# Performance work log

Hardware: AMD Instinct MI355X
Metric: run time of the kernel (lower is better)

Reference implementation:

```python
import jax, jax.numpy as jnp
import numpy as np

T, B, D, H = 1024, 512, 128, 256


def setup_inputs() -> dict:
    key = jax.random.key(0)
    k0, k1, k2, k3, k4, k5 = jax.random.split(key, 6)
    data = jax.random.normal(k0, (T, B, D), dtype=jnp.float32)
    # ragged lengths in [1, T]; masked recurrence == packed-sequence semantics
    lengths = jax.random.randint(k1, (B,), 1, T + 1, dtype=jnp.int32)
    s_ih = 1.0 / np.sqrt(D)
    s_hh = 1.0 / np.sqrt(H)
    ih_w = jax.random.uniform(k2, (H, D), minval=-s_ih, maxval=s_ih, dtype=jnp.float32)
    ih_b = jax.random.uniform(k3, (H,), minval=-s_ih, maxval=s_ih, dtype=jnp.float32)
    hh_w = jax.random.uniform(k4, (2 * H, H), minval=-s_hh, maxval=s_hh, dtype=jnp.float32)
    hh_b = jax.random.uniform(k5, (2 * H,), minval=-s_hh, maxval=s_hh, dtype=jnp.float32)
    return {"data": data, "ih_w": ih_w, "ih_b": ih_b, "hh_w": hh_w, "hh_b": hh_b, "lengths": lengths}


def reference(data, ih_w, ih_b, hh_w, hh_b, lengths):
    # data: [T, B, D]; masked update replicates packed-sequence 'first size rows' semantics
    Tn, Bn, _ = data.shape
    Hn = ih_w.shape[0]

    def step(hidden, inp):
        x_t, t = inp
        hid = hidden @ hh_w.T + hh_b                    # [B, 2H]
        alpha, h = jnp.split(hid, 2, axis=1)
        alpha = jax.nn.sigmoid(alpha)
        h = (jnp.exp2(alpha * h) - 1.0) / alpha + alpha  # soft-exp gate
        new_hidden = jnp.tanh(x_t @ ih_w.T + ih_b + h)   # [B, H]
        valid = (t < lengths)[:, None]
        return jnp.where(valid, new_hidden, hidden), None

    h0 = jnp.zeros((Bn, Hn), dtype=data.dtype)
    hidden, _ = jax.lax.scan(step, h0, (data, jnp.arange(Tn)))
    return hidden[None]  # [1, B, H], matching hidden.unsqueeze(0)
```

## Files before the change

kernel.cpp:

```cpp
#include <hip/hip_runtime.h>


#define BB 512
#define DD 128
#define HH 256

typedef __attribute__((ext_vector_type(8))) short bf16x8;
typedef __attribute__((ext_vector_type(4))) float f32x4;

static __device__ __forceinline__ short f2bf(float f) {
    unsigned u = __float_as_uint(f);
    u += 0x7FFFu + ((u >> 16) & 1u);
    return (short)(u >> 16);
}
static __device__ __forceinline__ float bf2f(short s) {
    return __uint_as_float(((unsigned)(unsigned short)s) << 16);
}
static __device__ __forceinline__ bf16x8 pack8(const float4 a, const float4 b) {
    bf16x8 v;
    v[0] = f2bf(a.x); v[1] = f2bf(a.y); v[2] = f2bf(a.z); v[3] = f2bf(a.w);
    v[4] = f2bf(b.x); v[5] = f2bf(b.y); v[6] = f2bf(b.z); v[7] = f2bf(b.w);
    return v;
}

__global__ __launch_bounds__(512, 2)
void rnn_fused(const float* __restrict__ data, const float* __restrict__ ih_w,
               const float* __restrict__ ih_b, const float* __restrict__ hh_w,
               const float* __restrict__ hh_b, const int* __restrict__ lengths,
               float* __restrict__ out)
{
    const int g    = blockIdx.x;
    const int tid  = threadIdx.x;
    const int w    = tid >> 6;
    const int lane = tid & 63;
    const int col  = lane & 15;
    const int quad = lane >> 4;

    __shared__ short hbuf[2][32][4][8];
    __shared__ short dbuf[2][2][DD];

    bf16x8 whh[4][8];
    #pragma unroll
    for (int s = 0; s < 2; ++s)
        #pragma unroll
        for (int j = 0; j < 2; ++j) {
            const int wrow = s*HH + 32*w + 16*j + col;
            const float* src = hh_w + wrow * HH;
            #pragma unroll
            for (int i = 0; i < 8; ++i) {
                const float4 a = *(const float4*)(src + i*32 + quad*8);
                const float4 b = *(const float4*)(src + i*32 + quad*8 + 4);
                whh[s*2 + j][i] = pack8(a, b);
            }
        }
    bf16x8 wih[2][4];
    #pragma unroll
    for (int j = 0; j < 2; ++j) {
        const int wrow = 32*w + 16*j + col;
        const float* src = ih_w + wrow * DD;
        #pragma unroll
        for (int i = 0; i < 4; ++i) {
            const float4 a = *(const float4*)(src + i*32 + quad*8);
            const float4 b = *(const float4*)(src + i*32 + quad*8 + 4);
            wih[j][i] = pack8(a, b);
        }
    }

    float bA[2], bH[2], bX[2];
    #pragma unroll
    for (int j = 0; j < 2; ++j) {
        bA[j] = hh_b[      32*w + 16*j + col];
        bH[j] = hh_b[HH  + 32*w + 16*j + col];
        bX[j] = ih_b[      32*w + 16*j + col];
    }

    const int L0 = lengths[2*g];
    const int L1 = lengths[2*g + 1];
    const int Lmax = (L0 > L1) ? L0 : L1;

    for (int idx = tid; idx < 32*4*8; idx += 512)
        ((short*)hbuf[0])[idx] = 0;
    if (tid < 256)
        ((short*)dbuf[0])[tid] = f2bf(data[(size_t)(2*g) * DD + tid]);
    float vstage = 0.f;
    if (tid < 256 && 1 < Lmax)
        vstage = data[((size_t)1 * BB + 2*g) * DD + tid];
    __syncthreads();

    float  nh[2][2] = {{0.f,0.f},{0.f,0.f}};
    bf16x8 af[4] = {};
    bf16x8 dh[4] = {};

    const bool act = (col < 4);

    for (int t = 0; t < Lmax; ++t) {
        const int p = t & 1;

        if (tid < 256 && t + 1 < Lmax)
            ((short*)dbuf[1 - p])[tid] = f2bf(vstage);
        float vnew = 0.f;
        if (tid < 256 && t + 2 < Lmax)
            vnew = data[((size_t)(t+2) * BB + 2*g) * DD + tid];

        f32x4 racc[4];
        #pragma unroll
        for (int j = 0; j < 2; ++j) {
            f32x4 va = {bA[j], bA[j], 0.f, 0.f}; racc[j]     = va;
            f32x4 vh = {bH[j], bH[j], 0.f, 0.f}; racc[2 + j] = vh;
        }
        #pragma unroll
        for (int half = 0; half < 2; ++half) {
            if (act) {
                #pragma unroll
                for (int i = 0; i < 4; ++i)
                    af[i] = *(const bf16x8*)
                        &hbuf[p][(half*4 + i)*4 + quad][col][0];
            }
            #pragma unroll
            for (int i = 0; i < 4; ++i)
                #pragma unroll
                for (int tt = 0; tt < 4; ++tt)
                    racc[tt] = __builtin_amdgcn_mfma_f32_16x16x32_bf16(
                        af[i], whh[tt][half*4 + i], racc[tt], 0, 0, 0);
        }

        if (act && col < 2) {
            #pragma unroll
            for (int i = 0; i < 4; ++i)
                dh[i] = *(const bf16x8*)&dbuf[p][col][i*32 + quad*8];
        }
        f32x4 xacc[2];
        #pragma unroll
        for (int j = 0; j < 2; ++j) {
            f32x4 v = {bX[j], bX[j], bX[j], bX[j]}; xacc[j] = v;
        }
        #pragma unroll
        for (int i = 0; i < 4; ++i)
            #pragma unroll
            for (int j = 0; j < 2; ++j)
                xacc[j] = __builtin_amdgcn_mfma_f32_16x16x32_bf16(
                    dh[i], wih[j][i], xacc[j], 0, 0, 0);

        #pragma unroll
        for (int j = 0; j < 2; ++j) {
            #pragma unroll
            for (int r = 0; r < 2; ++r) {
                const float a   = racc[j][r]     + racc[j][2 + r];
                const float hv  = racc[2 + j][r] + racc[2 + j][2 + r];
                const float e   = __builtin_amdgcn_exp2f(a * -1.4426950408889634f);
                const float inv = 1.0f + e;
                const float al  = __builtin_amdgcn_rcpf(inv);
                const float pp  = __builtin_amdgcn_exp2f(al * hv);
                const float gg  = (pp - 1.0f) * inv + al;
                const float u   = xacc[j][r] + gg;
                const float t2  = __builtin_amdgcn_exp2f(u * 2.8853900817779268f);
                const float th  = 1.0f - 2.0f * __builtin_amdgcn_rcpf(1.0f + t2);
                const int   Lr  = r ? L1 : L0;
                const float v   = (t < Lr) ? th : nh[j][r];
                nh[j][r] = v;
                if (quad == 0) {
                    const int   c  = 32*w + 16*j + col;
                    const short hi = f2bf(v);
                    const short lo = f2bf(v - bf2f(hi));
                    hbuf[1 - p][c >> 3][r    ][c & 7] = hi;
                    hbuf[1 - p][c >> 3][2 + r][c & 7] = lo;
                }
            }
        }

        vstage = vnew;
        __syncthreads();
    }

    if (quad == 0) {
        #pragma unroll
        for (int j = 0; j < 2; ++j)
            #pragma unroll
            for (int r = 0; r < 2; ++r)
                out[(size_t)(2*g + r) * HH + 32*w + 16*j + col] = nh[j][r];
    }
}

extern "C" void kernel_launch(void* const* d_in, const int* in_sizes, int n_in,
                              void* d_out, int out_size, void* d_ws, size_t ws_size,
                              hipStream_t stream) {
    const float* data    = (const float*)d_in[0];
    const float* ih_w    = (const float*)d_in[1];
    const float* ih_b    = (const float*)d_in[2];
    const float* hh_w    = (const float*)d_in[3];
    const float* hh_b    = (const float*)d_in[4];
    const int*   lengths = (const int*)d_in[5];
    float* out = (float*)d_out;

    (void)in_sizes; (void)n_in; (void)out_size; (void)d_ws; (void)ws_size;

    rnn_fused<<<dim3(BB / 2), dim3(512), 0, stream>>>(
        data, ih_w, ih_b, hh_w, hh_b, lengths, out);
}
```

Before: 1.474 ms.

## Split hidden columns across 16 waves per block to shorten per-step MFMA chain

Doubles the block size to 1024 threads so each wave owns 16 hidden columns instead of 32. This halves the per-wave recurrent and input MFMA counts and the gate math on the serial time-step critical path. Register weight storage per wave is halved, and biases are now added after accumulation. The cost is a barrier across more waves each step and higher register pressure on occupancy under the 1024,4 launch bound.

New measurement: 1.364 ms. 7.5% less time.

```diff
diff --git a/kernel.cpp b/kernel.cpp
--- a/kernel.cpp
+++ b/kernel.cpp
@@ -23,7 +23,7 @@
     return v;
 }
 
-__global__ __launch_bounds__(512, 2)
+__global__ __launch_bounds__(1024, 4)
 void rnn_fused(const float* __restrict__ data, const float* __restrict__ ih_w,
                const float* __restrict__ ih_b, const float* __restrict__ hh_w,
                const float* __restrict__ hh_b, const int* __restrict__ lengths,
@@ -39,46 +39,39 @@
     __shared__ short hbuf[2][32][4][8];
     __shared__ short dbuf[2][2][DD];
 
-    bf16x8 whh[4][8];
+    bf16x8 whh[2][8];
     #pragma unroll
-    for (int s = 0; s < 2; ++s)
+    for (int s = 0; s < 2; ++s) {
+        const int wrow = s*HH + 16*w + col;
+        const float* src = hh_w + wrow * HH;
         #pragma unroll
-        for (int j = 0; j < 2; ++j) {
-            const int wrow = s*HH + 32*w + 16*j + col;
-            const float* src = hh_w + wrow * HH;
-            #pragma unroll
-            for (int i = 0; i < 8; ++i) {
-                const float4 a = *(const float4*)(src + i*32 + quad*8);
-                const float4 b = *(const float4*)(src + i*32 + quad*8 + 4);
-                whh[s*2 + j][i] = pack8(a, b);
-            }
+        for (int i = 0; i < 8; ++i) {
+            const float4 a = *(const float4*)(src + i*32 + quad*8);
+            const float4 b = *(const float4*)(src + i*32 + quad*8 + 4);
+            whh[s][i] = pack8(a, b);
         }
-    bf16x8 wih[2][4];
-    #pragma unroll
-    for (int j = 0; j < 2; ++j) {
-        const int wrow = 32*w + 16*j + col;
+    }
+    bf16x8 wih[4];
+    {
+        const int wrow = 16*w + col;
         const float* src = ih_w + wrow * DD;
         #pragma unroll
         for (int i = 0; i < 4; ++i) {
             const float4 a = *(const float4*)(src + i*32 + quad*8);
             const float4 b = *(const float4*)(src + i*32 + quad*8 + 4);
-            wih[j][i] = pack8(a, b);
+            wih[i] = pack8(a, b);
         }
     }
 
-    float bA[2], bH[2], bX[2];
-    #pragma unroll
-    for (int j = 0; j < 2; ++j) {
-        bA[j] = hh_b[      32*w + 16*j + col];
-        bH[j] = hh_b[HH  + 32*w + 16*j + col];
-        bX[j] = ih_b[      32*w + 16*j + col];
-    }
+    const float bA = hh_b[      16*w + col];
+    const float bH = hh_b[HH  + 16*w + col];
+    const float bX = ih_b[      16*w + col];
 
     const int L0 = lengths[2*g];
     const int L1 = lengths[2*g + 1];
     const int Lmax = (L0 > L1) ? L0 : L1;
 
-    for (int idx = tid; idx < 32*4*8; idx += 512)
+    for (int idx = tid; idx < 32*4*8; idx += 1024)
         ((short*)hbuf[0])[idx] = 0;
     if (tid < 256)
         ((short*)dbuf[0])[tid] = f2bf(data[(size_t)(2*g) * DD + tid]);
@@ -87,11 +80,11 @@
         vstage = data[((size_t)1 * BB + 2*g) * DD + tid];
     __syncthreads();
 
-    float  nh[2][2] = {{0.f,0.f},{0.f,0.f}};
-    bf16x8 af[4] = {};
-    bf16x8 dh[4] = {};
+    float  nh[2] = {0.f, 0.f};
+    bf16x8 frag[4] = {};
 
-    const bool act = (col < 4);
+    const bool acth = (col < 4);
+    const bool actd = (col < 2);
 
     for (int t = 0; t < Lmax; ++t) {
         const int p = t & 1;
@@ -102,69 +95,55 @@
         if (tid < 256 && t + 2 < Lmax)
             vnew = data[((size_t)(t+2) * BB + 2*g) * DD + tid];
 
-        f32x4 racc[4];
-        #pragma unroll
-        for (int j = 0; j < 2; ++j) {
-            f32x4 va = {bA[j], bA[j], 0.f, 0.f}; racc[j]     = va;
-            f32x4 vh = {bH[j], bH[j], 0.f, 0.f}; racc[2 + j] = vh;
-        }
+        f32x4 racc[2] = {{0.f,0.f,0.f,0.f},{0.f,0.f,0.f,0.f}};
         #pragma unroll
         for (int half = 0; half < 2; ++half) {
-            if (act) {
+            if (acth) {
                 #pragma unroll
                 for (int i = 0; i < 4; ++i)
-                    af[i] = *(const bf16x8*)
+                    frag[i] = *(const bf16x8*)
                         &hbuf[p][(half*4 + i)*4 + quad][col][0];
             }
             #pragma unroll
             for (int i = 0; i < 4; ++i)
                 #pragma unroll
-                for (int tt = 0; tt < 4; ++tt)
-                    racc[tt] = __builtin_amdgcn_mfma_f32_16x16x32_bf16(
-                        af[i], whh[tt][half*4 + i], racc[tt], 0, 0, 0);
+                for (int s = 0; s < 2; ++s)
+                    racc[s] = __builtin_amdgcn_mfma_f32_16x16x32_bf16(
+                        frag[i], whh[s][half*4 + i], racc[s], 0, 0, 0);
         }
 
-        if (act && col < 2) {
+        if (actd) {
             #pragma unroll
             for (int i = 0; i < 4; ++i)
-                dh[i] = *(const bf16x8*)&dbuf[p][col][i*32 + quad*8];
+                frag[i] = *(const bf16x8*)&dbuf[p][col][i*32 + quad*8];
         }
-        f32x4 xacc[2];
-        #pragma unroll
-        for (int j = 0; j < 2; ++j) {
-            f32x4 v = {bX[j], bX[j], bX[j], bX[j]}; xacc[j] = v;
-        }
+        f32x4 xacc = {0.f, 0.f, 0.f, 0.f};
         #pragma unroll
         for (int i = 0; i < 4; ++i)
-            #pragma unroll
-            for (int j = 0; j < 2; ++j)
-                xacc[j] = __builtin_amdgcn_mfma_f32_16x16x32_bf16(
-                    dh[i], wih[j][i], xacc[j], 0, 0, 0);
+            xacc = __builtin_amdgcn_mfma_f32_16x16x32_bf16(
+                frag[i], wih[i], xacc, 0, 0, 0);
 
         #pragma unroll
-        for (int j = 0; j < 2; ++j) {
-            #pragma unroll
-            for (int r = 0; r < 2; ++r) {
-                const float a   = racc[j][r]     + racc[j][2 + r];
-                const float hv  = racc[2 + j][r] + racc[2 + j][2 + r];
-                const float e   = __builtin_amdgcn_exp2f(a * -1.4426950408889634f);
-                const float inv = 1.0f + e;
-                const float al  = __builtin_amdgcn_rcpf(inv);
-                const float pp  = __builtin_amdgcn_exp2f(al * hv);
-                const float gg  = (pp - 1.0f) * inv + al;
-                const float u   = xacc[j][r] + gg;
-                const float t2  = __builtin_amdgcn_exp2f(u * 2.8853900817779268f);
-                const float th  = 1.0f - 2.0f * __builtin_amdgcn_rcpf(1.0f + t2);
-                const int   Lr  = r ? L1 : L0;
-                const float v   = (t < Lr) ? th : nh[j][r];
-                nh[j][r] = v;
-                if (quad == 0) {
-                    const int   c  = 32*w + 16*j + col;
-                    const short hi = f2bf(v);
-                    const short lo = f2bf(v - bf2f(hi));
-                    hbuf[1 - p][c >> 3][r    ][c & 7] = hi;
-                    hbuf[1 - p][c >> 3][2 + r][c & 7] = lo;
-                }
+        for (int r = 0; r < 2; ++r) {
+            const float a   = racc[0][r] + racc[0][2 + r] + bA;
+            const float hv  = racc[1][r] + racc[1][2 + r] + bH;
+            const float e   = __builtin_amdgcn_exp2f(a * -1.4426950408889634f);
+            const float inv = 1.0f + e;
+            const float al  = __builtin_amdgcn_rcpf(inv);
+            const float pp  = __builtin_amdgcn_exp2f(al * hv);
+            const float gg  = (pp - 1.0f) * inv + al;
+            const float u   = xacc[r] + bX + gg;
+            const float t2  = __builtin_amdgcn_exp2f(u * 2.8853900817779268f);
+            const float th  = 1.0f - 2.0f * __builtin_amdgcn_rcpf(1.0f + t2);
+            const int   Lr  = r ? L1 : L0;
+            const float v   = (t < Lr) ? th : nh[r];
+            nh[r] = v;
+            if (quad == 0) {
+                const int   c  = 16*w + col;
+                const short hi = f2bf(v);
+                const short lo = f2bf(v - bf2f(hi));
+                hbuf[1 - p][c >> 3][r    ][c & 7] = hi;
+                hbuf[1 - p][c >> 3][2 + r][c & 7] = lo;
             }
         }
 
@@ -174,10 +153,8 @@
 
     if (quad == 0) {
         #pragma unroll
-        for (int j = 0; j < 2; ++j)
-            #pragma unroll
-            for (int r = 0; r < 2; ++r)
-                out[(size_t)(2*g + r) * HH + 32*w + 16*j + col] = nh[j][r];
+        for (int r = 0; r < 2; ++r)
+            out[(size_t)(2*g + r) * HH + 16*w + col] = nh[r];
     }
 }
 
@@ -194,6 +171,6 @@
 
     (void)in_sizes; (void)n_in; (void)out_size; (void)d_ws; (void)ws_size;
 
-    rnn_fused<<<dim3(BB / 2), dim3(512), 0, stream>>>(
+    rnn_fused<<<dim3(BB / 2), dim3(1024), 0, stream>>>(
         data, ih_w, ih_b, hh_w, hh_b, lengths, out);
 }
```
